# Kernel optimization log

Measured on AMD Instinct MI355X. Metric: run time of the kernel, lower is better.

Reference implementation:

```python
import jax, jax.numpy as jnp
import numpy as np

NUM_HEADS = 16


def setup_inputs() -> dict:
    key = jax.random.key(0)
    k1, k2, k3, k4, k5 = jax.random.split(key, 5)
    B, S, D = 4, 2048, 1024
    hidden_states = jax.random.normal(k1, (B, S, D), dtype=jnp.float32)
    c_attn_w = jax.random.normal(k2, (D, 3 * D), dtype=jnp.float32) * 0.02
    c_attn_b = jax.random.normal(k3, (3 * D,), dtype=jnp.float32) * 0.02
    c_proj_w = jax.random.normal(k4, (D, D), dtype=jnp.float32) * 0.02
    c_proj_b = jax.random.normal(k5, (D,), dtype=jnp.float32) * 0.02
    return {
        "hidden_states": hidden_states,
        "c_attn_w": c_attn_w,
        "c_attn_b": c_attn_b,
        "c_proj_w": c_proj_w,
        "c_proj_b": c_proj_b,
    }


def reference(hidden_states, c_attn_w, c_attn_b, c_proj_w, c_proj_b):
    B, S, D = hidden_states.shape
    H = NUM_HEADS
    Dh = D // H

    # fused QKV projection (Conv1D: x @ W + b)
    qkv = hidden_states @ c_attn_w + c_attn_b          # [B, S, 3D]
    q, k, v = jnp.split(qkv, 3, axis=-1)

    def split_heads(t):
        return t.reshape(B, S, H, Dh).transpose(0, 2, 1, 3)  # [B, H, S, Dh]

    q, k, v = split_heads(q), split_heads(k), split_heads(v)

    # scaled dot-product attention with causal mask (eager GPT2 _attn)
    scores = jnp.einsum("bhqd,bhkd->bhqk", q, k) / jnp.asarray(Dh ** 0.5, q.dtype)
    causal = jnp.tril(jnp.ones((S, S), dtype=bool))
    mask_value = jnp.finfo(scores.dtype).min
    scores = jnp.where(causal[None, None], scores, mask_value)
    probs = jax.nn.softmax(scores, axis=-1)            # attn_pdrop=0 -> no dropout
    attn = jnp.einsum("bhqk,bhkd->bhqd", probs, v)     # [B, H, S, Dh]

    # merge heads + output projection (resid_pdrop=0)
    attn = attn.transpose(0, 2, 1, 3).reshape(B, S, D)
    out = attn @ c_proj_w + c_proj_b
    return out
```

## Files before the change

### kernel.cpp

```cpp
#include <hip/hip_runtime.h>
#include <hip/hip_bf16.h>
#include <stdint.h>

typedef __bf16 bf16_t;
typedef __bf16 bf16x8 __attribute__((ext_vector_type(8)));
typedef __bf16 bf16x4 __attribute__((ext_vector_type(4)));
typedef float f32x4 __attribute__((ext_vector_type(4)));
typedef float f32x16 __attribute__((ext_vector_type(16)));

#define B_ 4
#define S_ 2048
#define D_ 1024
#define H_ 16
#define DH_ 64

__global__ __launch_bounds__(256) void cast_f32_to_bf16(const float* __restrict__ in,
                                                        bf16_t* __restrict__ out, int n4) {
  int i = blockIdx.x * 256 + threadIdx.x;
  if (i < n4) {
    const float4 v = reinterpret_cast<const float4*>(in)[i];
    bf16x4 o;
    o[0] = (bf16_t)v.x; o[1] = (bf16_t)v.y; o[2] = (bf16_t)v.z; o[3] = (bf16_t)v.w;
    reinterpret_cast<bf16x4*>(out)[i] = o;
  }
}

__global__ __launch_bounds__(256) void transpose_cast(const float* __restrict__ in,
                                                      bf16_t* __restrict__ out, int K, int N) {
  __shared__ float tile[32][33];
  const int bx = blockIdx.x * 32;
  const int by = blockIdx.y * 32;
  const int tx = threadIdx.x & 31;
  const int ty = threadIdx.x >> 5;
#pragma unroll
  for (int i = 0; i < 32; i += 8)
    tile[ty + i][tx] = in[(size_t)(by + ty + i) * N + bx + tx];
  __syncthreads();
#pragma unroll
  for (int i = 0; i < 32; i += 8)
    out[(size_t)(bx + ty + i) * K + by + tx] = (bf16_t)tile[tx][ty + i];
}

__device__ __forceinline__ void gload_lds16(const bf16_t* g, bf16_t* l) {
  __builtin_amdgcn_global_load_lds((const __attribute__((address_space(1))) void*)g,
                                   (__attribute__((address_space(3))) void*)l, 16, 0, 0);
}

template <int MODE>
__global__ __launch_bounds__(256) void gemm_bf16_128(
    const bf16_t* __restrict__ A, const bf16_t* __restrict__ Bt,
    const float* __restrict__ bias,
    bf16_t* __restrict__ Qb, bf16_t* __restrict__ Kb, bf16_t* __restrict__ Vtb,
    float* __restrict__ Out, int M, int N, int K) {
  __shared__ alignas(16) bf16_t As[128 * 32];
  __shared__ alignas(16) bf16_t Bs[128 * 32];
  const int t = threadIdx.x;
  const int wave = t >> 6, lane = t & 63;
  const int r = lane & 15, g = lane >> 4;
  const int bm = blockIdx.x, bn = blockIdx.y;
  const int wm = (wave & 1) * 64, wn = (wave >> 1) * 64;

  f32x4 acc[4][4];
#pragma unroll
  for (int i = 0; i < 4; ++i)
#pragma unroll
    for (int j = 0; j < 4; ++j) acc[i][j] = f32x4{0.f, 0.f, 0.f, 0.f};

  const int c0 = t;
  const int c1 = t + 256;

  for (int kk = 0; kk < K; kk += 32) {
    __syncthreads();
    gload_lds16(A + (size_t)(bm * 128 + (c0 >> 2)) * K + kk + (c0 & 3) * 8,
                As + (size_t)(wave * 64) * 8);
    gload_lds16(A + (size_t)(bm * 128 + (c1 >> 2)) * K + kk + (c1 & 3) * 8,
                As + (size_t)(256 + wave * 64) * 8);
    gload_lds16(Bt + (size_t)(bn * 128 + (c0 >> 2)) * K + kk + (c0 & 3) * 8,
                Bs + (size_t)(wave * 64) * 8);
    gload_lds16(Bt + (size_t)(bn * 128 + (c1 >> 2)) * K + kk + (c1 & 3) * 8,
                Bs + (size_t)(256 + wave * 64) * 8);
    __syncthreads();

    bf16x8 af[4], bfr[4];
#pragma unroll
    for (int f = 0; f < 4; ++f)
      af[f] = *reinterpret_cast<const bf16x8*>(&As[(wm + 16 * f + r) * 32 + g * 8]);
#pragma unroll
    for (int f = 0; f < 4; ++f)
      bfr[f] = *reinterpret_cast<const bf16x8*>(&Bs[(wn + 16 * f + r) * 32 + g * 8]);
#pragma unroll
    for (int fm = 0; fm < 4; ++fm)
#pragma unroll
      for (int fn = 0; fn < 4; ++fn)
        acc[fm][fn] =
            __builtin_amdgcn_mfma_f32_16x16x32_bf16(af[fm], bfr[fn], acc[fm][fn], 0, 0, 0);
  }

  const int row0 = bm * 128 + wm + g * 4;
  const int col0 = bn * 128 + wn + r;
#pragma unroll
  for (int fn = 0; fn < 4; ++fn) {
    const int col = col0 + 16 * fn;
    const float bv = bias[col];
    if (MODE == 0) {
      const int part = col >> 10, w = col & 1023;
      const int h = w >> 6, dh = w & 63;
#pragma unroll
      for (int fm = 0; fm < 4; ++fm) {
        const int row = row0 + 16 * fm;
        const int b = row >> 11, s = row & 2047;
        const size_t bhb = (size_t)(b * H_ + h);
        if (part == 2) {
          union { bf16_t hh[4]; uint2 u; } pk;
#pragma unroll
          for (int j = 0; j < 4; ++j) pk.hh[j] = (bf16_t)(acc[fm][fn][j] + bv);
          *reinterpret_cast<uint2*>(&Vtb[(bhb * DH_ + dh) * S_ + s]) = pk.u;
        } else {
          bf16_t* dst = (part == 0) ? Qb : Kb;
#pragma unroll
          for (int j = 0; j < 4; ++j)
            dst[(bhb * S_ + s + j) * DH_ + dh] = (bf16_t)(acc[fm][fn][j] + bv);
        }
      }
    } else {
#pragma unroll
      for (int fm = 0; fm < 4; ++fm)
#pragma unroll
        for (int j = 0; j < 4; ++j) {
          const int row = row0 + 16 * fm + j;
          Out[(size_t)row * N + col] = acc[fm][fn][j] + bv;
        }
    }
  }
}

__global__ __launch_bounds__(256) void attn_flash4(const bf16_t* __restrict__ Qb,
                                                   const bf16_t* __restrict__ Kb,
                                                   const bf16_t* __restrict__ Vtb,
                                                   bf16_t* __restrict__ attnb) {
  __shared__ alignas(16) bf16_t Kl[2][64 * 64];
  __shared__ alignas(16) bf16_t Vl[2][64 * 64];
  __shared__ alignas(16) bf16_t Ps[4][32 * 72];
  const int t = threadIdx.x, wave = t >> 6, lane = t & 63;
  const int q5 = lane & 31, hi = lane >> 5;
  const int bh = blockIdx.x, qb = 15 - (int)blockIdx.y;
  const size_t kqbase = (size_t)bh * (S_ * DH_);
  const size_t vbase = (size_t)bh * (DH_ * S_);
  const int b = bh >> 4, h = bh & 15;
  const float SC = 0.18033688f;

  const int r0s = t >> 3, ch0 = t & 7;
  const int r1s = (t + 256) >> 3, ch1 = t & 7;
  const int lk0 = r0s * 64 + ((ch0 ^ (r0s & 7)) << 3);
  const int lk1 = r1s * 64 + ((ch1 ^ (r1s & 7)) << 3);

  const int qbase = qb * 128;
  const int wq = qbase + wave * 32;
  const int qg = wq + q5;
  const int ktmax = 2 * qb + 1;
  const int ktw = wq >> 6;

  bf16x8 qf[4];
#pragma unroll
  for (int d = 0; d < 4; ++d)
    qf[d] = *reinterpret_cast<const bf16x8*>(Qb + kqbase + (size_t)qg * DH_ + d * 16 + hi * 8);

  f32x16 oa, ob;
#pragma unroll
  for (int r = 0; r < 16; ++r) { oa[r] = 0.f; ob[r] = 0.f; }
  float mrun = -1e30f, lrun = 0.f;

  {
    const bf16_t* kg = Kb + kqbase;
    const bf16_t* vg = Vtb + vbase;
    const uint4 a = *reinterpret_cast<const uint4*>(kg + r0s * DH_ + ch0 * 8);
    const uint4 bq = *reinterpret_cast<const uint4*>(kg + r1s * DH_ + ch1 * 8);
    const uint4 c = *reinterpret_cast<const uint4*>(vg + (size_t)r0s * S_ + ch0 * 8);
    const uint4 d = *reinterpret_cast<const uint4*>(vg + (size_t)r1s * S_ + ch1 * 8);
    *reinterpret_cast<uint4*>(&Kl[0][lk0]) = a;
    *reinterpret_cast<uint4*>(&Kl[0][lk1]) = bq;
    *reinterpret_cast<uint4*>(&Vl[0][lk0]) = c;
    *reinterpret_cast<uint4*>(&Vl[0][lk1]) = d;
    __syncthreads();
  }

  int cur = 0;
  for (int kt = 0; kt <= ktmax; ++kt) {
    uint4 ra, rb, rc, rd;
    const bool more = kt < ktmax;
    if (more) {
      const bf16_t* kg = Kb + kqbase + (size_t)(kt + 1) * (64 * DH_);
      const bf16_t* vg = Vtb + vbase + (kt + 1) * 64;
      ra = *reinterpret_cast<const uint4*>(kg + r0s * DH_ + ch0 * 8);
      rb = *reinterpret_cast<const uint4*>(kg + r1s * DH_ + ch1 * 8);
      rc = *reinterpret_cast<const uint4*>(vg + (size_t)r0s * S_ + ch0 * 8);
      rd = *reinterpret_cast<const uint4*>(vg + (size_t)r1s * S_ + ch1 * 8);
    }

    if (kt <= ktw) {
      const bf16_t* KL = &Kl[cur][0];
      const bf16_t* VL = &Vl[cur][0];
      f32x16 s0, s1;
#pragma unroll
      for (int r = 0; r < 16; ++r) { s0[r] = 0.f; s1[r] = 0.f; }
#pragma unroll
      for (int d = 0; d < 4; ++d) {
        const int cx = ((2 * d + hi) ^ (q5 & 7)) << 3;
        const bf16x8 kfa = *reinterpret_cast<const bf16x8*>(&KL[q5 * 64 + cx]);
        s0 = __builtin_amdgcn_mfma_f32_32x32x16_bf16(kfa, qf[d], s0, 0, 0, 0);
        const bf16x8 kfb = *reinterpret_cast<const bf16x8*>(&KL[(32 + q5) * 64 + cx]);
        s1 = __builtin_amdgcn_mfma_f32_32x32x16_bf16(kfb, qf[d], s1, 0, 0, 0);
      }

      if (kt == ktw) {
#pragma unroll
        for (int r = 0; r < 16; ++r) {
          const int crow = (r & 3) + 8 * (r >> 2) + 4 * hi;
          if (kt * 64 + crow > qg) s0[r] = -1e30f;
          if (kt * 64 + 32 + crow > qg) s1[r] = -1e30f;
        }
      }

      float t8[8];
#pragma unroll
      for (int i = 0; i < 8; ++i)
        t8[i] = fmaxf(fmaxf(s0[i], s0[i + 8]), fmaxf(s1[i], s1[i + 8]));
      float vm = fmaxf(fmaxf(fmaxf(t8[0], t8[1]), fmaxf(t8[2], t8[3])),
                       fmaxf(fmaxf(t8[4], t8[5]), fmaxf(t8[6], t8[7])));
      vm = fmaxf(vm, __shfl_xor(vm, 32));
      const float vms = vm * SC;

      if (!__all(vms - mrun <= 8.f)) {
        const float mnew = fmaxf(mrun, vms);
        const float fac = exp2f(mrun - mnew);
#pragma unroll
        for (int r = 0; r < 16; ++r) { oa[r] *= fac; ob[r] *= fac; }
        lrun *= fac;
        mrun = mnew;
      }

      float p0[16], p1[16];
#pragma unroll
      for (int r = 0; r < 16; ++r) {
        p0[r] = exp2f(fmaf(s0[r], SC, -mrun));
        p1[r] = exp2f(fmaf(s1[r], SC, -mrun));
      }
      float s8[8];
#pragma unroll
      for (int i = 0; i < 8; ++i) s8[i] = (p0[i] + p0[i + 8]) + (p1[i] + p1[i + 8]);
      float sum = ((s8[0] + s8[1]) + (s8[2] + s8[3])) + ((s8[4] + s8[5]) + (s8[6] + s8[7]));
      sum += __shfl_xor(sum, 32);
      lrun += sum;

      bf16_t* PSW = &Ps[wave][0];
#pragma unroll
      for (int r = 0; r < 16; r += 2) {
        const int crow = (r & 3) + 8 * (r >> 2) + 4 * hi;
        union { bf16_t hh[2]; unsigned u; } ua, ub;
        ua.hh[0] = (bf16_t)p0[r]; ua.hh[1] = (bf16_t)p0[r + 1];
        ub.hh[0] = (bf16_t)p1[r]; ub.hh[1] = (bf16_t)p1[r + 1];
        *reinterpret_cast<unsigned*>(&PSW[q5 * 72 + crow]) = ua.u;
        *reinterpret_cast<unsigned*>(&PSW[q5 * 72 + 32 + crow]) = ub.u;
      }

#pragma unroll
      for (int tt = 0; tt < 4; ++tt) {
        const bf16x8 pb = *reinterpret_cast<const bf16x8*>(&PSW[q5 * 72 + tt * 16 + hi * 8]);
        const int cx = ((2 * tt + hi) ^ (q5 & 7)) << 3;
        const bf16x8 va = *reinterpret_cast<const bf16x8*>(&VL[q5 * 64 + cx]);
        oa = __builtin_amdgcn_mfma_f32_32x32x16_bf16(va, pb, oa, 0, 0, 0);
        const bf16x8 vb = *reinterpret_cast<const bf16x8*>(&VL[(32 + q5) * 64 + cx]);
        ob = __builtin_amdgcn_mfma_f32_32x32x16_bf16(vb, pb, ob, 0, 0, 0);
      }
    }

    if (more) {
      *reinterpret_cast<uint4*>(&Kl[cur ^ 1][lk0]) = ra;
      *reinterpret_cast<uint4*>(&Kl[cur ^ 1][lk1]) = rb;
      *reinterpret_cast<uint4*>(&Vl[cur ^ 1][lk0]) = rc;
      *reinterpret_cast<uint4*>(&Vl[cur ^ 1][lk1]) = rd;
    }
    __syncthreads();
    cur ^= 1;
  }

  const float inv = 1.0f / lrun;
  bf16_t* PSW = &Ps[wave][0];
#pragma unroll
  for (int r = 0; r < 16; ++r) {
    const int crow = (r & 3) + 8 * (r >> 2) + 4 * hi;
    PSW[q5 * 72 + crow] = (bf16_t)(oa[r] * inv);
    PSW[q5 * 72 + 32 + crow] = (bf16_t)(ob[r] * inv);
  }
#pragma unroll
  for (int i = 0; i < 4; ++i) {
    const int cc = i * 64 + lane;
    const int row = cc >> 3, ch = cc & 7;
    const bf16x8 v = *reinterpret_cast<const bf16x8*>(&PSW[row * 72 + ch * 8]);
    *reinterpret_cast<bf16x8*>(attnb + ((size_t)(b * S_ + wq + row)) * D_ + h * DH_ + ch * 8) = v;
  }
}

extern "C" void kernel_launch(void* const* d_in, const int* in_sizes, int n_in, void* d_out,
                              int out_size, void* d_ws, size_t ws_size, hipStream_t stream) {
  const float* x = (const float*)d_in[0];
  const float* wqkv = (const float*)d_in[1];
  const float* bqkv = (const float*)d_in[2];
  const float* wproj = (const float*)d_in[3];
  const float* bproj = (const float*)d_in[4];
  float* out = (float*)d_out;
  char* ws = (char*)d_ws;

  bf16_t* xb = (bf16_t*)(ws);
  bf16_t* wqkvT = (bf16_t*)(ws + 16777216);
  bf16_t* wprojT = (bf16_t*)(ws + 23068672);
  bf16_t* Qb = (bf16_t*)(ws + 25165824);
  bf16_t* Kb = (bf16_t*)(ws + 41943040);
  bf16_t* Vtb = (bf16_t*)(ws + 58720256);
  bf16_t* attnb = (bf16_t*)(ws + 75497472);

  cast_f32_to_bf16<<<8192, 256, 0, stream>>>(x, xb, (8192 * 1024) / 4);
  transpose_cast<<<dim3(96, 32), 256, 0, stream>>>(wqkv, wqkvT, 1024, 3072);
  transpose_cast<<<dim3(32, 32), 256, 0, stream>>>(wproj, wprojT, 1024, 1024);
  gemm_bf16_128<0><<<dim3(64, 24), 256, 0, stream>>>(xb, wqkvT, bqkv, Qb, Kb, Vtb, nullptr,
                                                     8192, 3072, 1024);
  attn_flash4<<<dim3(64, 16), 256, 0, stream>>>(Qb, Kb, Vtb, attnb);
  gemm_bf16_128<1><<<dim3(64, 8), 256, 0, stream>>>(attnb, wprojT, bproj, nullptr, nullptr,
                                                    nullptr, out, 8192, 1024, 1024);
}
```

Baseline: 279.4 us.

## Feed softmax probabilities to PV MFMA from registers via permuted V layout

```diff
diff --git a/kernel.cpp b/kernel.cpp
--- a/kernel.cpp
+++ b/kernel.cpp
@@ -111,10 +111,11 @@
         const int b = row >> 11, s = row & 2047;
         const size_t bhb = (size_t)(b * H_ + h);
         if (part == 2) {
+          const int s2 = (s & ~12) | ((s & 4) << 1) | ((s & 8) >> 1);
           union { bf16_t hh[4]; uint2 u; } pk;
 #pragma unroll
           for (int j = 0; j < 4; ++j) pk.hh[j] = (bf16_t)(acc[fm][fn][j] + bv);
-          *reinterpret_cast<uint2*>(&Vtb[(bhb * DH_ + dh) * S_ + s]) = pk.u;
+          *reinterpret_cast<uint2*>(&Vtb[(bhb * DH_ + dh) * S_ + s2]) = pk.u;
         } else {
           bf16_t* dst = (part == 0) ? Qb : Kb;
 #pragma unroll
@@ -134,13 +135,11 @@
   }
 }
 
-__global__ __launch_bounds__(256) void attn_flash4(const bf16_t* __restrict__ Qb,
+__global__ __launch_bounds__(256) void attn_flash5(const bf16_t* __restrict__ Qb,
                                                    const bf16_t* __restrict__ Kb,
                                                    const bf16_t* __restrict__ Vtb,
                                                    bf16_t* __restrict__ attnb) {
-  __shared__ alignas(16) bf16_t Kl[2][64 * 64];
-  __shared__ alignas(16) bf16_t Vl[2][64 * 64];
-  __shared__ alignas(16) bf16_t Ps[4][32 * 72];
+  __shared__ alignas(16) bf16_t smem[4 * 64 * 64];
   const int t = threadIdx.x, wave = t >> 6, lane = t & 63;
   const int q5 = lane & 31, hi = lane >> 5;
   const int bh = blockIdx.x, qb = 15 - (int)blockIdx.y;
@@ -177,10 +176,10 @@
     const uint4 bq = *reinterpret_cast<const uint4*>(kg + r1s * DH_ + ch1 * 8);
     const uint4 c = *reinterpret_cast<const uint4*>(vg + (size_t)r0s * S_ + ch0 * 8);
     const uint4 d = *reinterpret_cast<const uint4*>(vg + (size_t)r1s * S_ + ch1 * 8);
-    *reinterpret_cast<uint4*>(&Kl[0][lk0]) = a;
-    *reinterpret_cast<uint4*>(&Kl[0][lk1]) = bq;
-    *reinterpret_cast<uint4*>(&Vl[0][lk0]) = c;
-    *reinterpret_cast<uint4*>(&Vl[0][lk1]) = d;
+    *reinterpret_cast<uint4*>(&smem[lk0]) = a;
+    *reinterpret_cast<uint4*>(&smem[lk1]) = bq;
+    *reinterpret_cast<uint4*>(&smem[8192 + lk0]) = c;
+    *reinterpret_cast<uint4*>(&smem[8192 + lk1]) = d;
     __syncthreads();
   }
 
@@ -198,8 +197,8 @@
     }
 
     if (kt <= ktw) {
-      const bf16_t* KL = &Kl[cur][0];
-      const bf16_t* VL = &Vl[cur][0];
+      const bf16_t* KL = smem + cur * 4096;
+      const bf16_t* VL = smem + 8192 + cur * 4096;
       f32x16 s0, s1;
 #pragma unroll
       for (int r = 0; r < 16; ++r) { s0[r] = 0.f; s1[r] = 0.f; }
@@ -252,40 +251,38 @@
       sum += __shfl_xor(sum, 32);
       lrun += sum;
 
-      bf16_t* PSW = &Ps[wave][0];
-#pragma unroll
-      for (int r = 0; r < 16; r += 2) {
-        const int crow = (r & 3) + 8 * (r >> 2) + 4 * hi;
-        union { bf16_t hh[2]; unsigned u; } ua, ub;
-        ua.hh[0] = (bf16_t)p0[r]; ua.hh[1] = (bf16_t)p0[r + 1];
-        ub.hh[0] = (bf16_t)p1[r]; ub.hh[1] = (bf16_t)p1[r + 1];
-        *reinterpret_cast<unsigned*>(&PSW[q5 * 72 + crow]) = ua.u;
-        *reinterpret_cast<unsigned*>(&PSW[q5 * 72 + 32 + crow]) = ub.u;
+      bf16x8 pbf[4];
+#pragma unroll
+      for (int i = 0; i < 8; ++i) {
+        pbf[0][i] = (bf16_t)p0[i];
+        pbf[1][i] = (bf16_t)p0[i + 8];
+        pbf[2][i] = (bf16_t)p1[i];
+        pbf[3][i] = (bf16_t)p1[i + 8];
       }
 
 #pragma unroll
       for (int tt = 0; tt < 4; ++tt) {
-        const bf16x8 pb = *reinterpret_cast<const bf16x8*>(&PSW[q5 * 72 + tt * 16 + hi * 8]);
         const int cx = ((2 * tt + hi) ^ (q5 & 7)) << 3;
         const bf16x8 va = *reinterpret_cast<const bf16x8*>(&VL[q5 * 64 + cx]);
-        oa = __builtin_amdgcn_mfma_f32_32x32x16_bf16(va, pb, oa, 0, 0, 0);
+        oa = __builtin_amdgcn_mfma_f32_32x32x16_bf16(va, pbf[tt], oa, 0, 0, 0);
         const bf16x8 vb = *reinterpret_cast<const bf16x8*>(&VL[(32 + q5) * 64 + cx]);
-        ob = __builtin_amdgcn_mfma_f32_32x32x16_bf16(vb, pb, ob, 0, 0, 0);
+        ob = __builtin_amdgcn_mfma_f32_32x32x16_bf16(vb, pbf[tt], ob, 0, 0, 0);
       }
     }
 
     if (more) {
-      *reinterpret_cast<uint4*>(&Kl[cur ^ 1][lk0]) = ra;
-      *reinterpret_cast<uint4*>(&Kl[cur ^ 1][lk1]) = rb;
-      *reinterpret_cast<uint4*>(&Vl[cur ^ 1][lk0]) = rc;
-      *reinterpret_cast<uint4*>(&Vl[cur ^ 1][lk1]) = rd;
+      const int nxt = (cur ^ 1) * 4096;
+      *reinterpret_cast<uint4*>(&smem[nxt + lk0]) = ra;
+      *reinterpret_cast<uint4*>(&smem[nxt + lk1]) = rb;
+      *reinterpret_cast<uint4*>(&smem[8192 + nxt + lk0]) = rc;
+      *reinterpret_cast<uint4*>(&smem[8192 + nxt + lk1]) = rd;
     }
     __syncthreads();
     cur ^= 1;
   }
 
   const float inv = 1.0f / lrun;
-  bf16_t* PSW = &Ps[wave][0];
+  bf16_t* PSW = smem + wave * 2304;
 #pragma unroll
   for (int r = 0; r < 16; ++r) {
     const int crow = (r & 3) + 8 * (r >> 2) + 4 * hi;
@@ -324,7 +321,7 @@
   transpose_cast<<<dim3(32, 32), 256, 0, stream>>>(wproj, wprojT, 1024, 1024);
   gemm_bf16_128<0><<<dim3(64, 24), 256, 0, stream>>>(xb, wqkvT, bqkv, Qb, Kb, Vtb, nullptr,
                                                      8192, 3072, 1024);
-  attn_flash4<<<dim3(64, 16), 256, 0, stream>>>(Qb, Kb, Vtb, attnb);
+  attn_flash5<<<dim3(64, 16), 256, 0, stream>>>(Qb, Kb, Vtb, attnb);
   gemm_bf16_128<1><<<dim3(64, 8), 256, 0, stream>>>(attnb, wprojT, bproj, nullptr, nullptr,
                                                     nullptr, out, 8192, 1024, 1024);
 }
```

After: 282.6 us. Within noise of the previous version (+1.1%).
